# Kernel optimization log

Hardware: AMD Instinct MI355X
Metric: run time of the kernel (lower is better)

## Reference

```python
import jax, jax.numpy as jnp
import numpy as np

B, S, C = 4, 2048, 1024
H = 16
D = C // H  # head_dim = 64


def setup_inputs() -> dict:
    key = jax.random.key(0)
    ks = jax.random.split(key, 5)
    scale = 0.02
    return {
        "x": jax.random.normal(ks[0], (B, S, C), dtype=jnp.float32),
        "qkv_w": jax.random.normal(ks[1], (3 * C, C), dtype=jnp.float32) * scale,
        "qkv_b": jax.random.normal(ks[2], (3 * C,), dtype=jnp.float32) * scale,
        "proj_w": jax.random.normal(ks[3], (C, C), dtype=jnp.float32) * scale,
        "proj_b": jax.random.normal(ks[4], (C,), dtype=jnp.float32) * scale,
    }


def reference(x, qkv_w, qkv_b, proj_w, proj_b):
    b, s, c = x.shape
    qkv = x @ qkv_w.T + qkv_b            # [b,s,3c] (torch Linear: x W^T + b)
    q, k, v = jnp.split(qkv, 3, axis=2)
    # [b,s,c] -> [b,h,s,d]
    def heads(t):
        return t.reshape(b, s, H, D).transpose(0, 2, 1, 3)
    q, k, v = heads(q), heads(k), heads(v)
    scores = jnp.einsum("bhqd,bhkd->bhqk", q, k) / jnp.sqrt(jnp.float32(D))
    causal = jnp.tril(jnp.ones((s, s), dtype=bool))
    scores = jnp.where(causal[None, None], scores, -jnp.inf)
    weights = jax.nn.softmax(scores, axis=-1)
    out = jnp.einsum("bhqk,bhkd->bhqd", weights, v)
    out = out.transpose(0, 2, 1, 3).reshape(b, s, c)
    return out @ proj_w.T + proj_b
```

## Files before the change

### kernel.cpp

```cpp
#include <hip/hip_runtime.h>
#include <hip/hip_bf16.h>


typedef __attribute__((ext_vector_type(8))) short short8;
typedef __attribute__((ext_vector_type(4))) float floatx4;

__device__ __forceinline__ unsigned short f2b(float f) {
    union { float f; unsigned u; } x; x.f = f;
    unsigned r = (x.u + 0x7fffu + ((x.u >> 16) & 1u)) >> 16;
    return (unsigned short)r;
}

__device__ __forceinline__ void load16_to_lds(const unsigned short* g, unsigned short* l) {
    auto gp = (const __attribute__((address_space(1))) unsigned int*)(unsigned long long)g;
    auto lp = (__attribute__((address_space(3))) unsigned int*)(unsigned int)(unsigned long long)l;
    __builtin_amdgcn_global_load_lds(gp, lp, 16, 0, 0);
}

__global__ void __launch_bounds__(256)
f32_to_bf16_vec(const float* __restrict__ in, unsigned short* __restrict__ out, int n4) {
    int i = blockIdx.x * blockDim.x + threadIdx.x;
    if (i < n4) {
        float4 f = ((const float4*)in)[i];
        ushort4 u;
        u.x = f2b(f.x); u.y = f2b(f.y); u.z = f2b(f.z); u.w = f2b(f.w);
        ((ushort4*)out)[i] = u;
    }
}

template<int MODE>
__global__ void __launch_bounds__(256)
gemm_nt(const unsigned short* __restrict__ A, const unsigned short* __restrict__ Bw,
        const float* __restrict__ bias, int M, int N, int K,
        unsigned short* __restrict__ Qo, unsigned short* __restrict__ Ko,
        unsigned short* __restrict__ Vo, float* __restrict__ Co) {
    __shared__ unsigned short As[128][64];
    __shared__ unsigned short Bs[128][64];
    const int tid = threadIdx.x;
    const int wave = tid >> 6, lane = tid & 63;
    const int lane15 = lane & 15, quad = lane >> 4;
    const int waveM = wave >> 1, waveN = wave & 1;
    const int m0 = blockIdx.y * 128, n0 = blockIdx.x * 128;
    const int swz = (lane15 & 7);

    floatx4 acc[4][4];
#pragma unroll
    for (int i = 0; i < 4; ++i)
#pragma unroll
        for (int j = 0; j < 4; ++j) acc[i][j] = (floatx4){0.f, 0.f, 0.f, 0.f};

    for (int kt = 0; kt < K; kt += 64) {
        __syncthreads();
#pragma unroll
        for (int i = 0; i < 4; ++i) {
            int idx = tid + i * 256;
            int r = idx >> 3, c = idx & 7;
            int gc = (c ^ (r & 7)) * 8;
            load16_to_lds(&A[(size_t)(m0 + r) * K + kt + gc], &As[0][0] + idx * 8);
            load16_to_lds(&Bw[(size_t)(n0 + r) * K + kt + gc], &Bs[0][0] + idx * 8);
        }
        __asm__ volatile("s_waitcnt vmcnt(0)" ::: "memory");
        __syncthreads();
#pragma unroll
        for (int ks = 0; ks < 2; ++ks) {
            short8 af[4], bfr[4];
#pragma unroll
            for (int i = 0; i < 4; ++i)
                af[i] = *(const short8*)&As[waveM * 64 + i * 16 + lane15][((ks * 4 + quad) ^ swz) * 8];
#pragma unroll
            for (int j = 0; j < 4; ++j)
                bfr[j] = *(const short8*)&Bs[waveN * 64 + j * 16 + lane15][((ks * 4 + quad) ^ swz) * 8];
#pragma unroll
            for (int i = 0; i < 4; ++i)
#pragma unroll
                for (int j = 0; j < 4; ++j)
                    acc[i][j] = __builtin_amdgcn_mfma_f32_16x16x32_bf16(af[i], bfr[j], acc[i][j], 0, 0, 0);
        }
    }

    const float QSCALE = 0.18033688011112042f;
#pragma unroll
    for (int i = 0; i < 4; ++i)
#pragma unroll
        for (int j = 0; j < 4; ++j)
#pragma unroll
            for (int r = 0; r < 4; ++r) {
                int m = m0 + waveM * 64 + i * 16 + quad * 4 + r;
                int n = n0 + waveN * 64 + j * 16 + lane15;
                float v = acc[i][j][r] + bias[n];
                if (MODE == 0) {
                    int sel = n >> 10;
                    int c = n & 1023;
                    int h = c >> 6, d = c & 63;
                    int b = m >> 11, s = m & 2047;
                    size_t bh = (size_t)(b * 16 + h);
                    if (sel == 0) {
                        Qo[(bh * 2048 + s) * 64 + d] = f2b(v * QSCALE);
                    } else if (sel == 1) {
                        Ko[(bh * 2048 + s) * 64 + d] = f2b(v);
                    } else {
                        Vo[(bh * 64 + d) * 2048 + s] = f2b(v);
                    }
                } else {
                    Co[(size_t)m * N + n] = v;
                }
            }
}

__global__ void __launch_bounds__(256, 2)
attn_kernel(const unsigned short* __restrict__ Q, const unsigned short* __restrict__ K,
            const unsigned short* __restrict__ V, unsigned short* __restrict__ O) {
    const int S = 2048, D = 64;
    __shared__ unsigned short Ks[2][64][64];
    __shared__ unsigned short Vt[2][64][64];
    __shared__ unsigned short Ps[4][32][72];

    const int bx = blockIdx.x;
    const int bh = blockIdx.y;
    const int tid = threadIdx.x;
    const int wave = tid >> 6, lane = tid & 63;
    const int lane15 = lane & 15, quad = lane >> 4;
    const int swz = (lane15 & 7);

    const unsigned short* Qb = Q + (size_t)bh * S * D;
    const unsigned short* Kb = K + (size_t)bh * S * D;
    const unsigned short* Vb = V + (size_t)bh * D * S;
    const int b = bh >> 4, h = bh & 15;

    for (int qi = 0; qi < 2; ++qi) {
        const int qb = qi ? bx : 15 - bx;
        const int q0 = qb * 128;
        const int ntiles = 2 * qb + 2;

        short8 qf[2][2];
#pragma unroll
        for (int mi = 0; mi < 2; ++mi) {
            int qrow = q0 + wave * 32 + mi * 16 + lane15;
#pragma unroll
            for (int ks = 0; ks < 2; ++ks)
                qf[mi][ks] = *(const short8*)&Qb[(size_t)qrow * D + ks * 32 + quad * 8];
        }

        floatx4 o[2][4];
        float l_i[2][4];
#pragma unroll
        for (int mi = 0; mi < 2; ++mi)
#pragma unroll
            for (int r = 0; r < 4; ++r) {
                o[mi][r] = (floatx4){0.f, 0.f, 0.f, 0.f};
                l_i[mi][r] = 0.f;
            }

        auto stage = [&](int buf, int kb) {
#pragma unroll
            for (int i = 0; i < 2; ++i) {
                int idx = tid + i * 256;
                int r = idx >> 3, c = idx & 7;
                int gc = (c ^ (r & 7)) * 8;
                load16_to_lds(&Kb[(size_t)(kb + r) * D + gc], &Ks[buf][0][0] + idx * 8);
                load16_to_lds(&Vb[(size_t)r * S + kb + gc], &Vt[buf][0][0] + idx * 8);
            }
        };

        __syncthreads();
        stage(0, 0);

        for (int kt = 0; kt < ntiles; ++kt) {
            const int cur = kt & 1;
            const int kb = kt * 64;
            __asm__ volatile("s_waitcnt vmcnt(0)" ::: "memory");
            __syncthreads();
            if (kt + 1 < ntiles) stage(1 - cur, kb + 64);

            floatx4 sa[2][4];
#pragma unroll
            for (int mi = 0; mi < 2; ++mi)
#pragma unroll
                for (int j = 0; j < 4; ++j) sa[mi][j] = (floatx4){0.f, 0.f, 0.f, 0.f};
#pragma unroll
            for (int j = 0; j < 4; ++j)
#pragma unroll
                for (int ks = 0; ks < 2; ++ks) {
                    short8 kf = *(const short8*)&Ks[cur][j * 16 + lane15][((ks * 4 + quad) ^ swz) * 8];
#pragma unroll
                    for (int mi = 0; mi < 2; ++mi)
                        sa[mi][j] = __builtin_amdgcn_mfma_f32_16x16x32_bf16(qf[mi][ks], kf, sa[mi][j], 0, 0, 0);
                }

            if (kb + 64 > q0) {
#pragma unroll
                for (int mi = 0; mi < 2; ++mi)
#pragma unroll
                    for (int j = 0; j < 4; ++j)
#pragma unroll
                        for (int r = 0; r < 4; ++r) {
                            int key = kb + j * 16 + lane15;
                            int qq = q0 + wave * 32 + mi * 16 + quad * 4 + r;
                            if (key > qq) sa[mi][j][r] = -1e30f;
                        }
            }

#pragma unroll
            for (int mi = 0; mi < 2; ++mi) {
#pragma unroll
                for (int j = 0; j < 4; ++j)
#pragma unroll
                    for (int r = 0; r < 4; ++r)
                        sa[mi][j][r] = __builtin_amdgcn_exp2f(sa[mi][j][r]);
#pragma unroll
                for (int r = 0; r < 4; ++r)
                    l_i[mi][r] += (sa[mi][0][r] + sa[mi][1][r]) + (sa[mi][2][r] + sa[mi][3][r]);
#pragma unroll
                for (int j = 0; j < 4; ++j)
#pragma unroll
                    for (int r = 0; r < 4; ++r)
                        Ps[wave][mi * 16 + quad * 4 + r][j * 16 + lane15] = f2b(sa[mi][j][r]);
            }
            __asm__ volatile("s_waitcnt lgkmcnt(0)" ::: "memory");

            short8 pf[2][2];
#pragma unroll
            for (int mi = 0; mi < 2; ++mi)
#pragma unroll
                for (int ks = 0; ks < 2; ++ks)
                    pf[mi][ks] = *(const short8*)&Ps[wave][mi * 16 + lane15][ks * 32 + quad * 8];

#pragma unroll
            for (int jd = 0; jd < 4; ++jd)
#pragma unroll
                for (int ks = 0; ks < 2; ++ks) {
                    short8 vf = *(const short8*)&Vt[cur][jd * 16 + lane15][((ks * 4 + quad) ^ swz) * 8];
#pragma unroll
                    for (int mi = 0; mi < 2; ++mi)
                        o[mi][jd] = __builtin_amdgcn_mfma_f32_16x16x32_bf16(pf[mi][ks], vf, o[mi][jd], 0, 0, 0);
                }
        }

#pragma unroll
        for (int mi = 0; mi < 2; ++mi)
#pragma unroll
            for (int off = 8; off >= 1; off >>= 1)
#pragma unroll
                for (int r = 0; r < 4; ++r) l_i[mi][r] += __shfl_xor(l_i[mi][r], off);

#pragma unroll
        for (int mi = 0; mi < 2; ++mi)
#pragma unroll
            for (int r = 0; r < 4; ++r) {
                int qq = q0 + wave * 32 + mi * 16 + quad * 4 + r;
                float inv = 1.0f / l_i[mi][r];
#pragma unroll
                for (int jd = 0; jd < 4; ++jd)
                    O[((size_t)(b * 2048 + qq)) * 1024 + h * 64 + jd * 16 + lane15] =
                        f2b(o[mi][jd][r] * inv);
            }
    }
}

extern "C" void kernel_launch(void* const* d_in, const int* in_sizes, int n_in,
                              void* d_out, int out_size, void* d_ws, size_t ws_size,
                              hipStream_t stream) {
    const float* x      = (const float*)d_in[0];
    const float* qkv_w  = (const float*)d_in[1];
    const float* qkv_b  = (const float*)d_in[2];
    const float* proj_w = (const float*)d_in[3];
    const float* proj_b = (const float*)d_in[4];
    float* out = (float*)d_out;

    const int B = 4, S = 2048, C = 1024, M = B * S;

    char* ws = (char*)d_ws;
    size_t off = 0;
    auto alloc = [&](size_t bytes) {
        void* p = ws + off;
        off += (bytes + 255) & ~(size_t)255;
        return p;
    };
    unsigned short* xb    = (unsigned short*)alloc((size_t)M * C * 2);
    unsigned short* wqkv  = (unsigned short*)alloc((size_t)3 * C * C * 2);
    unsigned short* wproj = (unsigned short*)alloc((size_t)C * C * 2);
    unsigned short* Qb    = (unsigned short*)alloc((size_t)M * C * 2);
    unsigned short* Kb    = (unsigned short*)alloc((size_t)M * C * 2);
    unsigned short* Vb    = (unsigned short*)alloc((size_t)M * C * 2);
    unsigned short* attn  = (unsigned short*)alloc((size_t)M * C * 2);

    {
        int n4 = M * C / 4;
        f32_to_bf16_vec<<<(n4 + 255) / 256, 256, 0, stream>>>(x, xb, n4);
    }
    {
        int n4 = 3 * C * C / 4;
        f32_to_bf16_vec<<<(n4 + 255) / 256, 256, 0, stream>>>(qkv_w, wqkv, n4);
    }
    {
        int n4 = C * C / 4;
        f32_to_bf16_vec<<<(n4 + 255) / 256, 256, 0, stream>>>(proj_w, wproj, n4);
    }

    gemm_nt<0><<<dim3(3 * C / 128, M / 128), 256, 0, stream>>>(
        xb, wqkv, qkv_b, M, 3 * C, C, Qb, Kb, Vb, nullptr);

    attn_kernel<<<dim3(8, B * 16), 256, 0, stream>>>(Qb, Kb, Vb, attn);

    gemm_nt<1><<<dim3(C / 128, M / 128), 256, 0, stream>>>(
        attn, wproj, proj_b, M, C, C, nullptr, nullptr, nullptr, out);
}
```

Before: 277.0 us.

## Keep softmax probabilities in registers via transposed MFMA and lane shuffles

The attention kernel now computes S transposed (K as the A operand), so each lane holds a query's scores along keys. The bf16 P fragment is then built with cross-lane shuffles instead of a round trip through LDS, and the Ps buffer is removed. The grid changes from 8 blocks, each processing a paired long and short query tile, to 16 blocks with one query tile each, and occupancy is raised to 3 blocks per CU. The three f32-to-bf16 conversion launches are merged into one, and output stores become 8-byte vector writes. The shuffles add VALU and permute work, and dropping the tile pairing leaves the causal workload per block unbalanced.

```diff
diff --git a/kernel.cpp b/kernel.cpp
--- a/kernel.cpp
+++ b/kernel.cpp
@@ -18,14 +18,19 @@
 }
 
 __global__ void __launch_bounds__(256)
-f32_to_bf16_vec(const float* __restrict__ in, unsigned short* __restrict__ out, int n4) {
-    int i = blockIdx.x * blockDim.x + threadIdx.x;
-    if (i < n4) {
-        float4 f = ((const float4*)in)[i];
-        ushort4 u;
-        u.x = f2b(f.x); u.y = f2b(f.y); u.z = f2b(f.z); u.w = f2b(f.w);
-        ((ushort4*)out)[i] = u;
-    }
+convert_all(const float* __restrict__ x, const float* __restrict__ w1,
+            const float* __restrict__ w2, unsigned short* __restrict__ xb,
+            unsigned short* __restrict__ wb1, unsigned short* __restrict__ wb2) {
+    const int N0 = 2097152, N1 = 786432;
+    int i = blockIdx.x * 256 + threadIdx.x;
+    const float* src; unsigned short* dst; int off;
+    if (i < N0)           { src = x;  dst = xb;  off = i; }
+    else if (i < N0 + N1) { src = w1; dst = wb1; off = i - N0; }
+    else                  { src = w2; dst = wb2; off = i - N0 - N1; }
+    float4 f = ((const float4*)src)[off];
+    ushort4 u;
+    u.x = f2b(f.x); u.y = f2b(f.y); u.z = f2b(f.z); u.w = f2b(f.w);
+    ((ushort4*)dst)[off] = u;
 }
 
 template<int MODE>
@@ -107,153 +112,164 @@
             }
 }
 
-__global__ void __launch_bounds__(256, 2)
+__global__ void __launch_bounds__(256, 3)
 attn_kernel(const unsigned short* __restrict__ Q, const unsigned short* __restrict__ K,
             const unsigned short* __restrict__ V, unsigned short* __restrict__ O) {
     const int S = 2048, D = 64;
     __shared__ unsigned short Ks[2][64][64];
     __shared__ unsigned short Vt[2][64][64];
-    __shared__ unsigned short Ps[4][32][72];
-
-    const int bx = blockIdx.x;
+
+    const int qb = 15 - blockIdx.x;
     const int bh = blockIdx.y;
     const int tid = threadIdx.x;
     const int wave = tid >> 6, lane = tid & 63;
     const int lane15 = lane & 15, quad = lane >> 4;
     const int swz = (lane15 & 7);
+    const int q0 = qb * 128;
+    const int ntiles = 2 * qb + 2;
 
     const unsigned short* Qb = Q + (size_t)bh * S * D;
     const unsigned short* Kb = K + (size_t)bh * S * D;
     const unsigned short* Vb = V + (size_t)bh * D * S;
     const int b = bh >> 4, h = bh & 15;
 
-    for (int qi = 0; qi < 2; ++qi) {
-        const int qb = qi ? bx : 15 - bx;
-        const int q0 = qb * 128;
-        const int ntiles = 2 * qb + 2;
-
-        short8 qf[2][2];
+    short8 qf[2][2];
+#pragma unroll
+    for (int mi = 0; mi < 2; ++mi) {
+        int qrow = q0 + wave * 32 + mi * 16 + lane15;
+#pragma unroll
+        for (int ks = 0; ks < 2; ++ks)
+            qf[mi][ks] = *(const short8*)&Qb[(size_t)qrow * D + ks * 32 + quad * 8];
+    }
+
+    floatx4 o[2][4];
+    float l_i[2] = {0.f, 0.f};
+#pragma unroll
+    for (int mi = 0; mi < 2; ++mi)
+#pragma unroll
+        for (int jd = 0; jd < 4; ++jd) o[mi][jd] = (floatx4){0.f, 0.f, 0.f, 0.f};
+
+    auto stage = [&](int buf, int kb) {
+#pragma unroll
+        for (int i = 0; i < 2; ++i) {
+            int idx = tid + i * 256;
+            int r = idx >> 3, c = idx & 7;
+            int gc = (c ^ (r & 7)) * 8;
+            load16_to_lds(&Kb[(size_t)(kb + r) * D + gc], &Ks[buf][0][0] + idx * 8);
+            load16_to_lds(&Vb[(size_t)r * S + kb + gc], &Vt[buf][0][0] + idx * 8);
+        }
+    };
+
+    stage(0, 0);
+
+    const int sl0 = lane15 + 16 * ((quad & 1) * 2);
+    const int sl1 = sl0 + 16;
+    const bool qhi = (quad >> 1) & 1;
+
+    for (int kt = 0; kt < ntiles; ++kt) {
+        const int cur = kt & 1;
+        const int kb = kt * 64;
+        __asm__ volatile("s_waitcnt vmcnt(0)" ::: "memory");
+        __syncthreads();
+        if (kt + 1 < ntiles) stage(1 - cur, kb + 64);
+
+        floatx4 sa[2][4];
+#pragma unroll
+        for (int mi = 0; mi < 2; ++mi)
+#pragma unroll
+            for (int j = 0; j < 4; ++j) sa[mi][j] = (floatx4){0.f, 0.f, 0.f, 0.f};
+#pragma unroll
+        for (int j = 0; j < 4; ++j)
+#pragma unroll
+            for (int ks = 0; ks < 2; ++ks) {
+                short8 kf = *(const short8*)&Ks[cur][j * 16 + lane15][((ks * 4 + quad) ^ swz) * 8];
+#pragma unroll
+                for (int mi = 0; mi < 2; ++mi)
+                    sa[mi][j] = __builtin_amdgcn_mfma_f32_16x16x32_bf16(kf, qf[mi][ks], sa[mi][j], 0, 0, 0);
+            }
+
+        if (kb + 64 > q0) {
+#pragma unroll
+            for (int mi = 0; mi < 2; ++mi)
+#pragma unroll
+                for (int j = 0; j < 4; ++j)
+#pragma unroll
+                    for (int r = 0; r < 4; ++r) {
+                        int key = kb + j * 16 + quad * 4 + r;
+                        int qq = q0 + wave * 32 + mi * 16 + lane15;
+                        if (key > qq) sa[mi][j][r] = -1e30f;
+                    }
+        }
+
+        unsigned pk[2][4][2];
 #pragma unroll
         for (int mi = 0; mi < 2; ++mi) {
-            int qrow = q0 + wave * 32 + mi * 16 + lane15;
-#pragma unroll
-            for (int ks = 0; ks < 2; ++ks)
-                qf[mi][ks] = *(const short8*)&Qb[(size_t)qrow * D + ks * 32 + quad * 8];
-        }
-
-        floatx4 o[2][4];
-        float l_i[2][4];
+            float part = 0.f;
+#pragma unroll
+            for (int j = 0; j < 4; ++j) {
+#pragma unroll
+                for (int r = 0; r < 4; ++r) {
+                    sa[mi][j][r] = __builtin_amdgcn_exp2f(sa[mi][j][r]);
+                    part += sa[mi][j][r];
+                }
+                pk[mi][j][0] = (unsigned)f2b(sa[mi][j][0]) | ((unsigned)f2b(sa[mi][j][1]) << 16);
+                pk[mi][j][1] = (unsigned)f2b(sa[mi][j][2]) | ((unsigned)f2b(sa[mi][j][3]) << 16);
+            }
+            l_i[mi] += part;
+        }
+
+        short8 pf[2][2];
 #pragma unroll
         for (int mi = 0; mi < 2; ++mi)
 #pragma unroll
-            for (int r = 0; r < 4; ++r) {
-                o[mi][r] = (floatx4){0.f, 0.f, 0.f, 0.f};
-                l_i[mi][r] = 0.f;
-            }
-
-        auto stage = [&](int buf, int kb) {
-#pragma unroll
-            for (int i = 0; i < 2; ++i) {
-                int idx = tid + i * 256;
-                int r = idx >> 3, c = idx & 7;
-                int gc = (c ^ (r & 7)) * 8;
-                load16_to_lds(&Kb[(size_t)(kb + r) * D + gc], &Ks[buf][0][0] + idx * 8);
-                load16_to_lds(&Vb[(size_t)r * S + kb + gc], &Vt[buf][0][0] + idx * 8);
-            }
-        };
-
-        __syncthreads();
-        stage(0, 0);
-
-        for (int kt = 0; kt < ntiles; ++kt) {
-            const int cur = kt & 1;
-            const int kb = kt * 64;
-            __asm__ volatile("s_waitcnt vmcnt(0)" ::: "memory");
-            __syncthreads();
-            if (kt + 1 < ntiles) stage(1 - cur, kb + 64);
-
-            floatx4 sa[2][4];
-#pragma unroll
-            for (int mi = 0; mi < 2; ++mi)
-#pragma unroll
-                for (int j = 0; j < 4; ++j) sa[mi][j] = (floatx4){0.f, 0.f, 0.f, 0.f};
-#pragma unroll
-            for (int j = 0; j < 4; ++j)
-#pragma unroll
-                for (int ks = 0; ks < 2; ++ks) {
-                    short8 kf = *(const short8*)&Ks[cur][j * 16 + lane15][((ks * 4 + quad) ^ swz) * 8];
-#pragma unroll
-                    for (int mi = 0; mi < 2; ++mi)
-                        sa[mi][j] = __builtin_amdgcn_mfma_f32_16x16x32_bf16(qf[mi][ks], kf, sa[mi][j], 0, 0, 0);
-                }
-
-            if (kb + 64 > q0) {
+            for (int ks = 0; ks < 2; ++ks) {
+                const int jl = ks * 2, jh = ks * 2 + 1;
+                unsigned a0 = (unsigned)__shfl((int)pk[mi][jl][0], sl0, 64);
+                unsigned b0 = (unsigned)__shfl((int)pk[mi][jh][0], sl0, 64);
+                unsigned a1 = (unsigned)__shfl((int)pk[mi][jl][1], sl0, 64);
+                unsigned b1 = (unsigned)__shfl((int)pk[mi][jh][1], sl0, 64);
+                unsigned a2 = (unsigned)__shfl((int)pk[mi][jl][0], sl1, 64);
+                unsigned b2 = (unsigned)__shfl((int)pk[mi][jh][0], sl1, 64);
+                unsigned a3 = (unsigned)__shfl((int)pk[mi][jl][1], sl1, 64);
+                unsigned b3 = (unsigned)__shfl((int)pk[mi][jh][1], sl1, 64);
+                union { short8 s8; unsigned u[4]; } t;
+                t.u[0] = qhi ? b0 : a0;
+                t.u[1] = qhi ? b1 : a1;
+                t.u[2] = qhi ? b2 : a2;
+                t.u[3] = qhi ? b3 : a3;
+                pf[mi][ks] = t.s8;
+            }
+
+#pragma unroll
+        for (int jd = 0; jd < 4; ++jd)
+#pragma unroll
+            for (int ks = 0; ks < 2; ++ks) {
+                short8 vf = *(const short8*)&Vt[cur][jd * 16 + lane15][((ks * 4 + quad) ^ swz) * 8];
 #pragma unroll
                 for (int mi = 0; mi < 2; ++mi)
-#pragma unroll
-                    for (int j = 0; j < 4; ++j)
-#pragma unroll
-                        for (int r = 0; r < 4; ++r) {
-                            int key = kb + j * 16 + lane15;
-                            int qq = q0 + wave * 32 + mi * 16 + quad * 4 + r;
-                            if (key > qq) sa[mi][j][r] = -1e30f;
-                        }
-            }
-
-#pragma unroll
-            for (int mi = 0; mi < 2; ++mi) {
-#pragma unroll
-                for (int j = 0; j < 4; ++j)
-#pragma unroll
-                    for (int r = 0; r < 4; ++r)
-                        sa[mi][j][r] = __builtin_amdgcn_exp2f(sa[mi][j][r]);
-#pragma unroll
-                for (int r = 0; r < 4; ++r)
-                    l_i[mi][r] += (sa[mi][0][r] + sa[mi][1][r]) + (sa[mi][2][r] + sa[mi][3][r]);
-#pragma unroll
-                for (int j = 0; j < 4; ++j)
-#pragma unroll
-                    for (int r = 0; r < 4; ++r)
-                        Ps[wave][mi * 16 + quad * 4 + r][j * 16 + lane15] = f2b(sa[mi][j][r]);
-            }
-            __asm__ volatile("s_waitcnt lgkmcnt(0)" ::: "memory");
-
-            short8 pf[2][2];
-#pragma unroll
-            for (int mi = 0; mi < 2; ++mi)
-#pragma unroll
-                for (int ks = 0; ks < 2; ++ks)
-                    pf[mi][ks] = *(const short8*)&Ps[wave][mi * 16 + lane15][ks * 32 + quad * 8];
-
-#pragma unroll
-            for (int jd = 0; jd < 4; ++jd)
-#pragma unroll
-                for (int ks = 0; ks < 2; ++ks) {
-                    short8 vf = *(const short8*)&Vt[cur][jd * 16 + lane15][((ks * 4 + quad) ^ swz) * 8];
-#pragma unroll
-                    for (int mi = 0; mi < 2; ++mi)
-                        o[mi][jd] = __builtin_amdgcn_mfma_f32_16x16x32_bf16(pf[mi][ks], vf, o[mi][jd], 0, 0, 0);
-                }
-        }
-
-#pragma unroll
-        for (int mi = 0; mi < 2; ++mi)
-#pragma unroll
-            for (int off = 8; off >= 1; off >>= 1)
-#pragma unroll
-                for (int r = 0; r < 4; ++r) l_i[mi][r] += __shfl_xor(l_i[mi][r], off);
-
-#pragma unroll
-        for (int mi = 0; mi < 2; ++mi)
-#pragma unroll
-            for (int r = 0; r < 4; ++r) {
-                int qq = q0 + wave * 32 + mi * 16 + quad * 4 + r;
-                float inv = 1.0f / l_i[mi][r];
-#pragma unroll
-                for (int jd = 0; jd < 4; ++jd)
-                    O[((size_t)(b * 2048 + qq)) * 1024 + h * 64 + jd * 16 + lane15] =
-                        f2b(o[mi][jd][r] * inv);
-            }
+                    o[mi][jd] = __builtin_amdgcn_mfma_f32_16x16x32_bf16(vf, pf[mi][ks], o[mi][jd], 0, 0, 0);
+            }
+    }
+
+#pragma unroll
+    for (int mi = 0; mi < 2; ++mi) {
+        l_i[mi] += __shfl_xor(l_i[mi], 16);
+        l_i[mi] += __shfl_xor(l_i[mi], 32);
+    }
+
+#pragma unroll
+    for (int mi = 0; mi < 2; ++mi) {
+        int qq = q0 + wave * 32 + mi * 16 + lane15;
+        float inv = 1.0f / l_i[mi];
+#pragma unroll
+        for (int jd = 0; jd < 4; ++jd) {
+            ushort4 w;
+            w.x = f2b(o[mi][jd][0] * inv);
+            w.y = f2b(o[mi][jd][1] * inv);
+            w.z = f2b(o[mi][jd][2] * inv);
+            w.w = f2b(o[mi][jd][3] * inv);
+            *(ushort4*)&O[((size_t)(b * 2048 + qq)) * 1024 + h * 64 + jd * 16 + quad * 4] = w;
+        }
     }
 }
 
@@ -285,22 +301,14 @@
     unsigned short* attn  = (unsigned short*)alloc((size_t)M * C * 2);
 
     {
-        int n4 = M * C / 4;
-        f32_to_bf16_vec<<<(n4 + 255) / 256, 256, 0, stream>>>(x, xb, n4);
-    }
-    {
-        int n4 = 3 * C * C / 4;
-        f32_to_bf16_vec<<<(n4 + 255) / 256, 256, 0, stream>>>(qkv_w, wqkv, n4);
-    }
-    {
-        int n4 = C * C / 4;
-        f32_to_bf16_vec<<<(n4 + 255) / 256, 256, 0, stream>>>(proj_w, wproj, n4);
+        int total4 = (M * C + 3 * C * C + C * C) / 4;
+        convert_all<<<total4 / 256, 256, 0, stream>>>(x, qkv_w, proj_w, xb, wqkv, wproj);
     }
 
     gemm_nt<0><<<dim3(3 * C / 128, M / 128), 256, 0, stream>>>(
         xb, wqkv, qkv_b, M, 3 * C, C, Qb, Kb, Vb, nullptr);
 
-    attn_kernel<<<dim3(8, B * 16), 256, 0, stream>>>(Qb, Kb, Vb, attn);
+    attn_kernel<<<dim3(16, B * 16), 256, 0, stream>>>(Qb, Kb, Vb, attn);
 
     gemm_nt<1><<<dim3(C / 128, M / 128), 256, 0, stream>>>(
         attn, wproj, proj_b, M, C, C, nullptr, nullptr, nullptr, out);
```

New measurement: 318.6 us. +15.0%, slower.
